# Kernel optimization log

Measured on AMD Instinct MI355X. Metric: run time of the kernel, lower is better.

The kernel has to match this reference:

```python
import math
import jax, jax.numpy as jnp
import numpy as np

D = 1536      # d_model
H = 12        # n_heads
L = 12        # n_layers
V = 50257     # vocab (hardcoded in module)
P = 1024      # max positions (hardcoded)
B = 1         # batch (must be 1: pos-embed uses arange(len(idx)))
S = 1024      # sequence length


def setup_inputs() -> dict:
    key = jax.random.key(0)
    ks = jax.random.split(key, 10)
    sc = 0.02
    n = lambda k, shape: (jax.random.normal(k, shape, jnp.float32) * sc)
    return {
        "idx": jax.random.randint(ks[0], (B, S), 0, V),
        "mask": jnp.tril(jnp.ones((S, S), jnp.int32)),  # causal mask
        "tok_emb": n(ks[1], (V, D)),
        "pos_emb": n(ks[2], (P, D)),
        "Wqkv": n(ks[3], (L, D, 3 * D)), "bqkv": jnp.zeros((L, 3 * D), jnp.float32),
        "Wo":   n(ks[4], (L, D, D)),     "bo":   jnp.zeros((L, D), jnp.float32),
        "W1":   n(ks[5], (L, D, 4 * D)), "b1":   jnp.zeros((L, 4 * D), jnp.float32),
        "W2":   n(ks[6], (L, 4 * D, D)), "b2":   jnp.zeros((L, D), jnp.float32),
        "ln_g": jnp.ones((D,), jnp.float32), "ln_b": jnp.zeros((D,), jnp.float32),
        "Wout": n(ks[7], (D, D)), "bout": jnp.zeros((D,), jnp.float32),
    }


def _gpt_forward(idx, mask, tok_emb, pos_emb, Wqkv, bqkv, Wo, bo,
                 W1, b1, W2, b2, ln_g, ln_b, Wout, bout):
    b, s = idx.shape
    d = tok_emb.shape[1]
    hd = d // H
    scale = 1.0 / math.sqrt(d)  # note: module divides by sqrt(d_model), not head_dim

    # faithful quirk: position_embedding(arange(len(idx))) -> (B, D), broadcasts since B==1
    x = tok_emb[idx] + pos_emb[:b]  # (B,S,D)

    mask0 = (mask == 0)  # (S,S) -> broadcast over (B,H,S,S)

    def block(x, p):
        wqkv, bqkv_, wo, bo_, w1, b1_, w2, b2_ = p
        qkv = x @ wqkv + bqkv_                       # (B,S,3D)
        q, k, v = jnp.split(qkv, 3, axis=-1)
        q = q.reshape(b, s, H, hd)
        k = k.reshape(b, s, H, hd)
        v = v.reshape(b, s, H, hd)
        scores = jnp.einsum('bqhd,bkhd->bhqk', q, k) * scale
        scores = jnp.where(mask0, -jnp.inf, scores)
        attn = jax.nn.softmax(scores, axis=-2)       # non-standard: softmax over QUERY axis
        o = jnp.einsum('bhqk,bkhd->bqhd', attn, v).reshape(b, s, d)
        x = x + (o @ wo + bo_)                       # attention residual
        x = x + (jax.nn.relu(x @ w1 + b1_) @ w2 + b2_)  # FFN residual (on post-attn x)
        return x, None

    x, _ = jax.lax.scan(block, x, (Wqkv, bqkv, Wo, bo, W1, b1, W2, b2))

    # final LayerNorm (eps=1e-5 like torch default)
    mu = jnp.mean(x, axis=-1, keepdims=True)
    var = jnp.mean(jnp.square(x - mu), axis=-1, keepdims=True)
    xn = (x - mu) * jax.lax.rsqrt(var + 1e-5) * ln_g + ln_b
    return xn @ Wout + bout


def reference(idx, mask, tok_emb, pos_emb, Wqkv, bqkv, Wo, bo,
              W1, b1, W2, b2, ln_g, ln_b, Wout, bout):
    return _gpt_forward(idx, mask, tok_emb, pos_emb, Wqkv, bqkv, Wo, bo,
                        W1, b1, W2, b2, ln_g, ln_b, Wout, bout)
```

## Files before the change

### kernel.cpp

```cpp
#include <hip/hip_runtime.h>
#include <stdint.h>
#include <math.h>

#define D_MODEL 1536
#define NH 12
#define HD 128
#define NL 12
#define SEQ 1024
#define D3 4608
#define D4 6144
#define SCALE 0.025515518153991442f

typedef __attribute__((ext_vector_type(8))) short short8;
typedef __attribute__((ext_vector_type(4))) float floatx4;

__device__ __forceinline__ uint32_t packhi(float a, float b) {
  return (__float_as_uint(a) >> 16) | (__float_as_uint(b) & 0xFFFF0000u);
}
__device__ __forceinline__ float truncf32(float a) {
  return __uint_as_float(__float_as_uint(a) & 0xFFFF0000u);
}
__device__ __forceinline__ void split8v(float4 v0, float4 v1, uint4 &hi, uint4 &lo) {
  hi.x = packhi(v0.x, v0.y); hi.y = packhi(v0.z, v0.w);
  hi.z = packhi(v1.x, v1.y); hi.w = packhi(v1.z, v1.w);
  lo.x = packhi(v0.x - truncf32(v0.x), v0.y - truncf32(v0.y));
  lo.y = packhi(v0.z - truncf32(v0.z), v0.w - truncf32(v0.w));
  lo.z = packhi(v1.x - truncf32(v1.x), v1.y - truncf32(v1.y));
  lo.w = packhi(v1.z - truncf32(v1.z), v1.w - truncf32(v1.w));
}

__device__ __forceinline__ int xcd_chunk_id(int nwg) {
  int orig = blockIdx.x;
  int xcd = orig & 7, pos = orig >> 3;
  int q = nwg >> 3, r = nwg & 7;
  return (xcd < r ? xcd * (q + 1) : r * (q + 1) + (xcd - r) * q) + pos;
}

__global__ __launch_bounds__(256)
void embed_kernel(const int* __restrict__ idx, const float* __restrict__ tok,
                  const float* __restrict__ pos, float* __restrict__ x) {
  int i = blockIdx.x * 256 + threadIdx.x;
  int s = i / D_MODEL;
  int d = i - s * D_MODEL;
  x[i] = tok[(size_t)idx[s] * D_MODEL + d] + pos[d];
}

template<int BM, bool RELU, bool RES, int SPLITK, bool TA2>
__global__ __launch_bounds__(256)
void mgemm_kernel(const float* __restrict__ A, const float* __restrict__ Ab,
                  const float* __restrict__ B,
                  const float* __restrict__ bias, const float* __restrict__ res,
                  float* __restrict__ C, int M, int N, int K, int NC, int NR) {
  constexpr int MI = BM / 32;
  constexpr int AE = BM / 8;
  constexpr int TPR = 32 / AE;
  __shared__ short Ah[2][BM][36], Al[2][BM][36];
  __shared__ short Bh[2][128][36], Bl[2][128][36];
  const int tid = threadIdx.x;
  const int lane = tid & 63, wave = tid >> 6;

  const int lid = xcd_chunk_id(NC * NR * SPLITK);
  const int z   = lid / (NC * NR);
  const int rem = lid - z * (NC * NR);
  const int ct  = rem / NR;
  const int rt  = rem - ct * NR;
  const int bm = rt * BM, bn = ct << 7;

  const int wm = (wave >> 1) * (BM / 2), wn = (wave & 1) << 6;
  const int fr = lane & 15, fk = (lane >> 4) << 3;
  const int Kc = K / SPLITK;
  const int kbase = (SPLITK > 1) ? z * Kc : 0;

  floatx4 acc[MI][4];
#pragma unroll
  for (int i = 0; i < MI; i++)
#pragma unroll
    for (int j = 0; j < 4; j++) acc[i][j] = (floatx4){0.f, 0.f, 0.f, 0.f};

  const int ar = tid / TPR;
  const int ac = (tid % TPR) * AE;
  const int bc = tid & 127;
  const int bkq = (tid >> 7) << 4;
  const float* Ag  = A + (size_t)(bm + ar) * K + kbase + ac;
  const float* Ag2 = TA2 ? (Ab + (size_t)(bm + ar) * K + kbase + ac) : nullptr;
  const float* Bg = B + (size_t)(kbase + bkq) * N + bn + bc;

  float a_reg[AE];
  float b_reg[16];

  auto LOADG = [&](int k0) {
#pragma unroll
    for (int e = 0; e < AE / 4; e++) {
      float4 v = *(const float4*)(Ag + k0 + 4 * e);
      if constexpr (TA2) {
        float4 w = *(const float4*)(Ag2 + k0 + 4 * e);
        v.x += w.x; v.y += w.y; v.z += w.z; v.w += w.w;
      }
      a_reg[4 * e + 0] = v.x; a_reg[4 * e + 1] = v.y;
      a_reg[4 * e + 2] = v.z; a_reg[4 * e + 3] = v.w;
    }
    const float* Bp = Bg + (size_t)k0 * N;
#pragma unroll
    for (int j = 0; j < 16; j++) b_reg[j] = Bp[(size_t)j * N];
  };
  auto STORE = [&](int buf) {
#pragma unroll
    for (int e = 0; e < AE / 8; e++) {
      float4 v0 = {a_reg[8 * e + 0], a_reg[8 * e + 1], a_reg[8 * e + 2], a_reg[8 * e + 3]};
      float4 v1 = {a_reg[8 * e + 4], a_reg[8 * e + 5], a_reg[8 * e + 6], a_reg[8 * e + 7]};
      uint4 hi, lo; split8v(v0, v1, hi, lo);
      *(uint4*)&Ah[buf][ar][ac + 8 * e] = hi;
      *(uint4*)&Al[buf][ar][ac + 8 * e] = lo;
    }
#pragma unroll
    for (int e = 0; e < 2; e++) {
      float4 u0 = {b_reg[8 * e + 0], b_reg[8 * e + 1], b_reg[8 * e + 2], b_reg[8 * e + 3]};
      float4 u1 = {b_reg[8 * e + 4], b_reg[8 * e + 5], b_reg[8 * e + 6], b_reg[8 * e + 7]};
      uint4 hi, lo; split8v(u0, u1, hi, lo);
      *(uint4*)&Bh[buf][bc][bkq + 8 * e] = hi;
      *(uint4*)&Bl[buf][bc][bkq + 8 * e] = lo;
    }
  };

  LOADG(0);
  STORE(0);
  __syncthreads();

  for (int k0 = 0; k0 < Kc; k0 += 32) {
    const int cur = (k0 >> 5) & 1;
    const bool more = (k0 + 32 < Kc);
    if (more) LOADG(k0 + 32);

    short8 ah[MI], al[MI], bh[4], bl[4];
#pragma unroll
    for (int i = 0; i < MI; i++) {
      ah[i] = *(const short8*)&Ah[cur][wm + (i << 4) + fr][fk];
      al[i] = *(const short8*)&Al[cur][wm + (i << 4) + fr][fk];
    }
#pragma unroll
    for (int j = 0; j < 4; j++) {
      bh[j] = *(const short8*)&Bh[cur][wn + (j << 4) + fr][fk];
      bl[j] = *(const short8*)&Bl[cur][wn + (j << 4) + fr][fk];
    }
#pragma unroll
    for (int i = 0; i < MI; i++)
#pragma unroll
      for (int j = 0; j < 4; j++) {
        acc[i][j] = __builtin_amdgcn_mfma_f32_16x16x32_bf16(ah[i], bh[j], acc[i][j], 0, 0, 0);
        acc[i][j] = __builtin_amdgcn_mfma_f32_16x16x32_bf16(ah[i], bl[j], acc[i][j], 0, 0, 0);
        acc[i][j] = __builtin_amdgcn_mfma_f32_16x16x32_bf16(al[i], bh[j], acc[i][j], 0, 0, 0);
      }

    if (more) STORE(cur ^ 1);
    __syncthreads();
  }

  const int cr = (lane >> 4) << 2, cc = lane & 15;
  if constexpr (SPLITK > 1) {
    float* Cp = C + (size_t)z * M * N;
#pragma unroll
    for (int j = 0; j < 4; j++) {
      const int col = bn + wn + (j << 4) + cc;
#pragma unroll
      for (int i = 0; i < MI; i++) {
        const int row0 = bm + wm + (i << 4) + cr;
#pragma unroll
        for (int r = 0; r < 4; r++)
          Cp[(size_t)(row0 + r) * N + col] = acc[i][j][r];
      }
    }
  } else {
#pragma unroll
    for (int j = 0; j < 4; j++) {
      const int col = bn + wn + (j << 4) + cc;
      const float bv = bias[col];
#pragma unroll
      for (int i = 0; i < MI; i++) {
        const int row0 = bm + wm + (i << 4) + cr;
#pragma unroll
        for (int r = 0; r < 4; r++) {
          float v = acc[i][j][r] + bv;
          if constexpr (RES) v += res[(size_t)(row0 + r) * N + col];
          if constexpr (RELU) v = fmaxf(v, 0.f);
          C[(size_t)(row0 + r) * N + col] = v;
        }
      }
    }
  }
}

template<bool HASB, bool RES, bool RELU>
__global__ __launch_bounds__(256)
void combine_kernel(const float* __restrict__ p0, const float* __restrict__ p1,
                    const float* __restrict__ bias, const float* __restrict__ res,
                    float* __restrict__ C, int N) {
  const int i = (blockIdx.x * 256 + threadIdx.x) << 2;
  float4 a = *(const float4*)&p0[i];
  float4 b = *(const float4*)&p1[i];
  float4 r = {a.x + b.x, a.y + b.y, a.z + b.z, a.w + b.w};
  if constexpr (HASB) {
    const int col = i % N;
    float4 bv = *(const float4*)&bias[col];
    r.x += bv.x; r.y += bv.y; r.z += bv.z; r.w += bv.w;
  }
  if constexpr (RES) {
    float4 rv = *(const float4*)&res[i];
    r.x += rv.x; r.y += rv.y; r.z += rv.z; r.w += rv.w;
  }
  if constexpr (RELU) {
    r.x = fmaxf(r.x, 0.f); r.y = fmaxf(r.y, 0.f);
    r.z = fmaxf(r.z, 0.f); r.w = fmaxf(r.w, 0.f);
  }
  *(float4*)&C[i] = r;
}

__global__ __launch_bounds__(256)
void scores_kernel(const float* __restrict__ qkv, float* __restrict__ scores,
                   float* __restrict__ pstats) {
  __shared__ short Qh[128][40], Ql[128][40], Kh[128][40], Kl[128][40];
  const int tid = threadIdx.x;
  const int lane = tid & 63, wave = tid >> 6;

  const int lid = xcd_chunk_id(NH * 36);
  const int h = lid / 36;
  int t = lid - h * 36;
  int rr = 0;
  while ((rr + 1) * (rr + 2) / 2 <= t) rr++;
  const int bi = rr << 7;
  const int bj = (t - rr * (rr + 1) / 2) << 7;

  const int wm = (wave >> 1) << 6, wn = (wave & 1) << 6;
  const int fr = lane & 15, fk = (lane >> 4) << 3;
  const float* Q = qkv + h * HD;
  const float* Kp = qkv + D_MODEL + h * HD;

  floatx4 acc[4][4];
#pragma unroll
  for (int i = 0; i < 4; i++)
#pragma unroll
    for (int j = 0; j < 4; j++) acc[i][j] = (floatx4){0.f, 0.f, 0.f, 0.f};

  const int ar = tid >> 1;
  const int ac = (tid & 1) << 4;

  for (int k0 = 0; k0 < HD; k0 += 32) {
    __syncthreads();
    {
      const float* Qp = Q + (size_t)(bi + ar) * D3 + k0 + ac;
#pragma unroll
      for (int e = 0; e < 2; e++) {
        float4 v0 = *(const float4*)(Qp + 8 * e);
        float4 v1 = *(const float4*)(Qp + 8 * e + 4);
        uint4 hi, lo; split8v(v0, v1, hi, lo);
        *(uint4*)&Qh[ar][ac + 8 * e] = hi;
        *(uint4*)&Ql[ar][ac + 8 * e] = lo;
      }
      const float* Kpp = Kp + (size_t)(bj + ar) * D3 + k0 + ac;
#pragma unroll
      for (int e = 0; e < 2; e++) {
        float4 v0 = *(const float4*)(Kpp + 8 * e);
        float4 v1 = *(const float4*)(Kpp + 8 * e + 4);
        uint4 hi, lo; split8v(v0, v1, hi, lo);
        *(uint4*)&Kh[ar][ac + 8 * e] = hi;
        *(uint4*)&Kl[ar][ac + 8 * e] = lo;
      }
    }
    __syncthreads();
    short8 qh[4], ql[4], kh[4], kl[4];
#pragma unroll
    for (int i = 0; i < 4; i++) {
      qh[i] = *(const short8*)&Qh[wm + (i << 4) + fr][fk];
      ql[i] = *(const short8*)&Ql[wm + (i << 4) + fr][fk];
      kh[i] = *(const short8*)&Kh[wn + (i << 4) + fr][fk];
      kl[i] = *(const short8*)&Kl[wn + (i << 4) + fr][fk];
    }
#pragma unroll
    for (int i = 0; i < 4; i++)
#pragma unroll
      for (int j = 0; j < 4; j++) {
        acc[i][j] = __builtin_amdgcn_mfma_f32_16x16x32_bf16(qh[i], kh[j], acc[i][j], 0, 0, 0);
        acc[i][j] = __builtin_amdgcn_mfma_f32_16x16x32_bf16(qh[i], kl[j], acc[i][j], 0, 0, 0);
        acc[i][j] = __builtin_amdgcn_mfma_f32_16x16x32_bf16(ql[i], kh[j], acc[i][j], 0, 0, 0);
        acc[i][j] = __builtin_amdgcn_mfma_f32_16x16x32_bf16(ql[i], kl[j], acc[i][j], 0, 0, 0);
      }
  }

  const int cr = (lane >> 4) << 2, cc = lane & 15;
  float* S = scores + (size_t)h * SEQ * SEQ;
  const int qc = (bi >> 6) + (wave >> 1);
  float* Pm = pstats + (size_t)((h * 16 + qc) * 2 + 0) * 1024;
  float* Pz = pstats + (size_t)((h * 16 + qc) * 2 + 1) * 1024;
#pragma unroll
  for (int j = 0; j < 4; j++) {
    const int col = bj + wn + (j << 4) + cc;
    float vv[16];
    float m = -1e30f;
#pragma unroll
    for (int i = 0; i < 4; i++) {
      const int row0 = bi + wm + (i << 4) + cr;
#pragma unroll
      for (int r = 0; r < 4; r++) {
        float v = (col <= row0 + r) ? acc[i][j][r] * SCALE : -1e30f;
        S[(size_t)(row0 + r) * SEQ + col] = v;
        vv[i * 4 + r] = v;
        m = fmaxf(m, v);
      }
    }
    float zz = 0.f;
#pragma unroll
    for (int t2 = 0; t2 < 16; t2++) zz += __expf(vv[t2] - m);
    if (m == -1e30f) zz = 0.f;
#pragma unroll
    for (int off = 16; off <= 32; off <<= 1) {
      float mo = __shfl_xor(m, off, 64);
      float zo = __shfl_xor(zz, off, 64);
      float mn = fmaxf(m, mo);
      zz = zz * __expf(m - mn) + zo * __expf(mo - mn);
      m = mn;
    }
    if ((lane >> 4) == 0) { Pm[col] = m; Pz[col] = zz; }
  }
}

__global__ __launch_bounds__(256)
void av_kernel(const float* __restrict__ qkv, const float* __restrict__ scores,
               const float* __restrict__ pstats, float* __restrict__ part) {
  __shared__ short Ph[64][40], Pl[64][40], Vh[128][40], Vl[128][40];
  __shared__ float Ms[512], Rs[512];
  const int tid = threadIdx.x;
  const int lane = tid & 63, wave = tid >> 6;

  const int lid = xcd_chunk_id(NH * 32);
  const int h = lid >> 5;
  const int t = lid & 31;
  const int y = t >> 1, z = t & 1;
  const int bm = y << 6;

  const int wm = (wave >> 1) << 5, wn = (wave & 1) << 6;
  const int fr = lane & 15, fk = (lane >> 4) << 3;
  const float* S = scores + (size_t)h * SEQ * SEQ;
  const float* V = qkv + 2 * D_MODEL + h * HD;

  const int kbeg = z * (y + 1) * 32;
  const int kend = (z + 1) * (y + 1) * 32;
  const int ncols = kend - kbeg;

  for (int c0 = tid; c0 < ncols; c0 += 256) {
    const int c = kbeg + c0;
    const int q0 = c >> 6;
    float m = -1e30f;
    for (int qc = q0; qc < 16; qc++)
      m = fmaxf(m, pstats[(size_t)((h * 16 + qc) * 2 + 0) * 1024 + c]);
    float zz = 0.f;
    for (int qc = q0; qc < 16; qc++) {
      float pm = pstats[(size_t)((h * 16 + qc) * 2 + 0) * 1024 + c];
      float pz = pstats[(size_t)((h * 16 + qc) * 2 + 1) * 1024 + c];
      zz += pz * __expf(pm - m);
    }
    Ms[c0] = m;
    Rs[c0] = 1.f / zz;
  }

  floatx4 acc[2][4];
#pragma unroll
  for (int i = 0; i < 2; i++)
#pragma unroll
    for (int j = 0; j < 4; j++) acc[i][j] = (floatx4){0.f, 0.f, 0.f, 0.f};

  const int ar = tid >> 2;
  const int ac = (tid & 3) << 3;
  const int bc = tid & 127;
  const int bkq = (tid >> 7) << 4;

  for (int k0 = kbeg; k0 < kend; k0 += 32) {
    __syncthreads();
    {
      const float* Sp = S + (size_t)(bm + ar) * SEQ + k0 + ac;
      float4 v0 = *(const float4*)(Sp);
      float4 v1 = *(const float4*)(Sp + 4);
      float t8[8] = {v0.x, v0.y, v0.z, v0.w, v1.x, v1.y, v1.z, v1.w};
      float4 p0, p1;
      {
        int kk = k0 - kbeg + ac;
        p0.x = __expf(t8[0] - Ms[kk + 0]) * Rs[kk + 0];
        p0.y = __expf(t8[1] - Ms[kk + 1]) * Rs[kk + 1];
        p0.z = __expf(t8[2] - Ms[kk + 2]) * Rs[kk + 2];
        p0.w = __expf(t8[3] - Ms[kk + 3]) * Rs[kk + 3];
        p1.x = __expf(t8[4] - Ms[kk + 4]) * Rs[kk + 4];
        p1.y = __expf(t8[5] - Ms[kk + 5]) * Rs[kk + 5];
        p1.z = __expf(t8[6] - Ms[kk + 6]) * Rs[kk + 6];
        p1.w = __expf(t8[7] - Ms[kk + 7]) * Rs[kk + 7];
      }
      uint4 hi, lo; split8v(p0, p1, hi, lo);
      *(uint4*)&Ph[ar][ac] = hi;
      *(uint4*)&Pl[ar][ac] = lo;
    }
    {
      const float* Vp = V + (size_t)(k0 + bkq) * D3 + bc;
#pragma unroll
      for (int e = 0; e < 2; e++) {
        float4 u0, u1;
        u0.x = Vp[(size_t)(8 * e + 0) * D3]; u0.y = Vp[(size_t)(8 * e + 1) * D3];
        u0.z = Vp[(size_t)(8 * e + 2) * D3]; u0.w = Vp[(size_t)(8 * e + 3) * D3];
        u1.x = Vp[(size_t)(8 * e + 4) * D3]; u1.y = Vp[(size_t)(8 * e + 5) * D3];
        u1.z = Vp[(size_t)(8 * e + 6) * D3]; u1.w = Vp[(size_t)(8 * e + 7) * D3];
        uint4 hi, lo; split8v(u0, u1, hi, lo);
        *(uint4*)&Vh[bc][bkq + 8 * e] = hi;
        *(uint4*)&Vl[bc][bkq + 8 * e] = lo;
      }
    }
    __syncthreads();
    short8 ph[2], pl[2], vh[4], vl[4];
#pragma unroll
    for (int i = 0; i < 2; i++) {
      ph[i] = *(const short8*)&Ph[wm + (i << 4) + fr][fk];
      pl[i] = *(const short8*)&Pl[wm + (i << 4) + fr][fk];
    }
#pragma unroll
    for (int j = 0; j < 4; j++) {
      vh[j] = *(const short8*)&Vh[wn + (j << 4) + fr][fk];
      vl[j] = *(const short8*)&Vl[wn + (j << 4) + fr][fk];
    }
#pragma unroll
    for (int i = 0; i < 2; i++)
#pragma unroll
      for (int j = 0; j < 4; j++) {
        acc[i][j] = __builtin_amdgcn_mfma_f32_16x16x32_bf16(ph[i], vh[j], acc[i][j], 0, 0, 0);
        acc[i][j] = __builtin_amdgcn_mfma_f32_16x16x32_bf16(ph[i], vl[j], acc[i][j], 0, 0, 0);
        acc[i][j] = __builtin_amdgcn_mfma_f32_16x16x32_bf16(pl[i], vh[j], acc[i][j], 0, 0, 0);
      }
  }

  const int cr = (lane >> 4) << 2, cc = lane & 15;
  float* Cp = part + (size_t)z * SEQ * D_MODEL;
#pragma unroll
  for (int j = 0; j < 4; j++) {
    const int col = h * HD + wn + (j << 4) + cc;
#pragma unroll
    for (int i = 0; i < 2; i++) {
      const int row0 = bm + wm + (i << 4) + cr;
#pragma unroll
      for (int r = 0; r < 4; r++)
        Cp[(size_t)(row0 + r) * D_MODEL + col] = acc[i][j][r];
    }
  }
}

__global__ __launch_bounds__(256)
void ln_kernel(const float* __restrict__ x, const float* __restrict__ g,
               const float* __restrict__ bb, float* __restrict__ y) {
  __shared__ float red[8];
  const int row = blockIdx.x;
  const float* xr = x + (size_t)row * D_MODEL;
  float v[6];
  float s = 0.f, sq = 0.f;
#pragma unroll
  for (int i = 0; i < 6; i++) {
    v[i] = xr[256 * i + threadIdx.x];
    s += v[i];
    sq += v[i] * v[i];
  }
#pragma unroll
  for (int off = 32; off >= 1; off >>= 1) {
    s += __shfl_down(s, off, 64);
    sq += __shfl_down(sq, off, 64);
  }
  const int lane = threadIdx.x & 63, w = threadIdx.x >> 6;
  if (lane == 0) { red[w] = s; red[4 + w] = sq; }
  __syncthreads();
  if (threadIdx.x == 0) {
    red[0] = red[0] + red[1] + red[2] + red[3];
    red[4] = red[4] + red[5] + red[6] + red[7];
  }
  __syncthreads();
  const float mu = red[0] * (1.f / D_MODEL);
  const float var = red[4] * (1.f / D_MODEL) - mu * mu;
  const float rs = rsqrtf(var + 1e-5f);
#pragma unroll
  for (int i = 0; i < 6; i++) {
    int c = 256 * i + threadIdx.x;
    y[(size_t)row * D_MODEL + c] = (v[i] - mu) * rs * g[c] + bb[c];
  }
}

extern "C" void kernel_launch(void* const* d_in, const int* in_sizes, int n_in,
                              void* d_out, int out_size, void* d_ws, size_t ws_size,
                              hipStream_t stream) {
  (void)in_sizes; (void)n_in; (void)out_size; (void)ws_size;
  const int*   idx     = (const int*)d_in[0];
  const float* tok_emb = (const float*)d_in[2];
  const float* pos_emb = (const float*)d_in[3];
  const float* Wqkv    = (const float*)d_in[4];
  const float* bqkv    = (const float*)d_in[5];
  const float* Wo      = (const float*)d_in[6];
  const float* bo      = (const float*)d_in[7];
  const float* W1      = (const float*)d_in[8];
  const float* b1      = (const float*)d_in[9];
  const float* W2      = (const float*)d_in[10];
  const float* b2      = (const float*)d_in[11];
  const float* ln_g    = (const float*)d_in[12];
  const float* ln_b    = (const float*)d_in[13];
  const float* Wout    = (const float*)d_in[14];
  const float* bout    = (const float*)d_in[15];
  float* out = (float*)d_out;

  char* ws = (char*)d_ws;
  float* x      = (float*)(ws);
  float* qkv    = (float*)(ws + 6291456);
  float* pstats = (float*)(ws + 25165824);
  float* part   = (float*)(ws + 26836992);
  float* U      = (float*)(ws + 52002816);
  float* scores = U;
  float* h1     = U;
  float* xn     = U;
  const size_t PN = (size_t)SEQ * D_MODEL;

  embed_kernel<<<6144, 256, 0, stream>>>(idx, tok_emb, pos_emb, x);

  for (int l = 0; l < NL; l++) {
    const float* wqkv = Wqkv + (size_t)l * D_MODEL * D3;
    const float* bq   = bqkv + (size_t)l * D3;
    const float* wo   = Wo   + (size_t)l * D_MODEL * D_MODEL;
    const float* bo_  = bo   + (size_t)l * D_MODEL;
    const float* w1   = W1   + (size_t)l * D_MODEL * D4;
    const float* b1_  = b1   + (size_t)l * D4;
    const float* w2   = W2   + (size_t)l * D4 * D_MODEL;
    const float* b2_  = b2   + (size_t)l * D_MODEL;

    mgemm_kernel<128, false, false, 1, false><<<288, 256, 0, stream>>>(
        x, nullptr, wqkv, bq, nullptr, qkv, SEQ, D3, D_MODEL, 36, 8);
    scores_kernel<<<432, 256, 0, stream>>>(qkv, scores, pstats);
    av_kernel<<<384, 256, 0, stream>>>(qkv, scores, pstats, part);
    mgemm_kernel<64, false, false, 2, true><<<384, 256, 0, stream>>>(
        part, part + PN, wo, nullptr, nullptr, part + 2 * PN,
        SEQ, D_MODEL, D_MODEL, 12, 16);
    combine_kernel<true, true, false><<<1536, 256, 0, stream>>>(
        part + 2 * PN, part + 3 * PN, bo_, x, x, D_MODEL);
    mgemm_kernel<128, true, false, 1, false><<<384, 256, 0, stream>>>(
        x, nullptr, w1, b1_, nullptr, h1, SEQ, D4, D_MODEL, 48, 8);
    mgemm_kernel<64, false, false, 2, false><<<384, 256, 0, stream>>>(
        h1, nullptr, w2, nullptr, nullptr, part, SEQ, D_MODEL, D4, 12, 16);
    combine_kernel<true, true, false><<<1536, 256, 0, stream>>>(
        part, part + PN, b2_, x, x, D_MODEL);
  }

  ln_kernel<<<SEQ, 256, 0, stream>>>(x, ln_g, ln_b, xn);
  mgemm_kernel<64, false, false, 2, false><<<384, 256, 0, stream>>>(
      xn, nullptr, Wout, nullptr, nullptr, part, SEQ, D_MODEL, D_MODEL, 12, 16);
  combine_kernel<true, false, false><<<1536, 256, 0, stream>>>(
      part, part + PN, bout, nullptr, out, D_MODEL);
}
```

Measured before the change: 5.060 ms.

## Load A/Q/K/P MFMA fragments directly from global into registers, bypassing LDS

In the GEMM, scores and AV kernels, the row-major operand (A, Q/K, P) is now read from global memory straight into the per-lane MFMA fragment layout and split into bf16 hi/lo in registers, removing the LDS staging buffers. The scores kernel drops its barriers entirely. This saves shared-memory traffic, LDS capacity and syncs. In exchange, each wave redundantly loads A rows that other waves also need, and the global access pattern becomes less coalesced (16 rows by 32 bytes per fragment), which leans on L1/L2 hit rates.

```diff
diff --git a/kernel.cpp b/kernel.cpp
--- a/kernel.cpp
+++ b/kernel.cpp
@@ -28,6 +28,9 @@
   lo.z = packhi(v1.x - truncf32(v1.x), v1.y - truncf32(v1.y));
   lo.w = packhi(v1.z - truncf32(v1.z), v1.w - truncf32(v1.w));
 }
+__device__ __forceinline__ short8 u4s8(uint4 u) {
+  union { uint4 u; short8 s; } x; x.u = u; return x.s;
+}
 
 __device__ __forceinline__ int xcd_chunk_id(int nwg) {
   int orig = blockIdx.x;
@@ -52,9 +55,6 @@
                   const float* __restrict__ bias, const float* __restrict__ res,
                   float* __restrict__ C, int M, int N, int K, int NC, int NR) {
   constexpr int MI = BM / 32;
-  constexpr int AE = BM / 8;
-  constexpr int TPR = 32 / AE;
-  __shared__ short Ah[2][BM][36], Al[2][BM][36];
   __shared__ short Bh[2][128][36], Bl[2][128][36];
   const int tid = threadIdx.x;
   const int lane = tid & 63, wave = tid >> 6;
@@ -77,41 +77,27 @@
 #pragma unroll
     for (int j = 0; j < 4; j++) acc[i][j] = (floatx4){0.f, 0.f, 0.f, 0.f};
 
-  const int ar = tid / TPR;
-  const int ac = (tid % TPR) * AE;
   const int bc = tid & 127;
   const int bkq = (tid >> 7) << 4;
-  const float* Ag  = A + (size_t)(bm + ar) * K + kbase + ac;
-  const float* Ag2 = TA2 ? (Ab + (size_t)(bm + ar) * K + kbase + ac) : nullptr;
   const float* Bg = B + (size_t)(kbase + bkq) * N + bn + bc;
-
-  float a_reg[AE];
   float b_reg[16];
 
-  auto LOADG = [&](int k0) {
-#pragma unroll
-    for (int e = 0; e < AE / 4; e++) {
-      float4 v = *(const float4*)(Ag + k0 + 4 * e);
-      if constexpr (TA2) {
-        float4 w = *(const float4*)(Ag2 + k0 + 4 * e);
-        v.x += w.x; v.y += w.y; v.z += w.z; v.w += w.w;
-      }
-      a_reg[4 * e + 0] = v.x; a_reg[4 * e + 1] = v.y;
-      a_reg[4 * e + 2] = v.z; a_reg[4 * e + 3] = v.w;
-    }
+  const float* Aq[MI];
+  const float* Aq2[MI];
+#pragma unroll
+  for (int i = 0; i < MI; i++) {
+    Aq[i] = A + (size_t)(bm + wm + 16 * i + fr) * K + kbase + fk;
+    if constexpr (TA2) Aq2[i] = Ab + (size_t)(bm + wm + 16 * i + fr) * K + kbase + fk;
+  }
+
+  float4 a0c[MI], a1c[MI], a0n[MI], a1n[MI];
+
+  auto LOADB = [&](int k0) {
     const float* Bp = Bg + (size_t)k0 * N;
 #pragma unroll
     for (int j = 0; j < 16; j++) b_reg[j] = Bp[(size_t)j * N];
   };
-  auto STORE = [&](int buf) {
-#pragma unroll
-    for (int e = 0; e < AE / 8; e++) {
-      float4 v0 = {a_reg[8 * e + 0], a_reg[8 * e + 1], a_reg[8 * e + 2], a_reg[8 * e + 3]};
-      float4 v1 = {a_reg[8 * e + 4], a_reg[8 * e + 5], a_reg[8 * e + 6], a_reg[8 * e + 7]};
-      uint4 hi, lo; split8v(v0, v1, hi, lo);
-      *(uint4*)&Ah[buf][ar][ac + 8 * e] = hi;
-      *(uint4*)&Al[buf][ar][ac + 8 * e] = lo;
-    }
+  auto STOREB = [&](int buf) {
 #pragma unroll
     for (int e = 0; e < 2; e++) {
       float4 u0 = {b_reg[8 * e + 0], b_reg[8 * e + 1], b_reg[8 * e + 2], b_reg[8 * e + 3]};
@@ -121,21 +107,39 @@
       *(uint4*)&Bl[buf][bc][bkq + 8 * e] = lo;
     }
   };
-
-  LOADG(0);
-  STORE(0);
+  auto LOADA = [&](int k0, float4* d0, float4* d1) {
+#pragma unroll
+    for (int i = 0; i < MI; i++) {
+      float4 v0 = *(const float4*)(Aq[i] + k0);
+      float4 v1 = *(const float4*)(Aq[i] + k0 + 4);
+      if constexpr (TA2) {
+        float4 w0 = *(const float4*)(Aq2[i] + k0);
+        float4 w1 = *(const float4*)(Aq2[i] + k0 + 4);
+        v0.x += w0.x; v0.y += w0.y; v0.z += w0.z; v0.w += w0.w;
+        v1.x += w1.x; v1.y += w1.y; v1.z += w1.z; v1.w += w1.w;
+      }
+      d0[i] = v0; d1[i] = v1;
+    }
+  };
+
+  LOADB(0);
+  STOREB(0);
+  LOADA(0, a0c, a1c);
   __syncthreads();
 
   for (int k0 = 0; k0 < Kc; k0 += 32) {
     const int cur = (k0 >> 5) & 1;
     const bool more = (k0 + 32 < Kc);
-    if (more) LOADG(k0 + 32);
+    if (more) {
+      LOADB(k0 + 32);
+      LOADA(k0 + 32, a0n, a1n);
+    }
 
     short8 ah[MI], al[MI], bh[4], bl[4];
 #pragma unroll
     for (int i = 0; i < MI; i++) {
-      ah[i] = *(const short8*)&Ah[cur][wm + (i << 4) + fr][fk];
-      al[i] = *(const short8*)&Al[cur][wm + (i << 4) + fr][fk];
+      uint4 hi, lo; split8v(a0c[i], a1c[i], hi, lo);
+      ah[i] = u4s8(hi); al[i] = u4s8(lo);
     }
 #pragma unroll
     for (int j = 0; j < 4; j++) {
@@ -151,7 +155,11 @@
         acc[i][j] = __builtin_amdgcn_mfma_f32_16x16x32_bf16(al[i], bh[j], acc[i][j], 0, 0, 0);
       }
 
-    if (more) STORE(cur ^ 1);
+    if (more) {
+      STOREB(cur ^ 1);
+#pragma unroll
+      for (int i = 0; i < MI; i++) { a0c[i] = a0n[i]; a1c[i] = a1n[i]; }
+    }
     __syncthreads();
   }
 
@@ -217,7 +225,6 @@
 __global__ __launch_bounds__(256)
 void scores_kernel(const float* __restrict__ qkv, float* __restrict__ scores,
                    float* __restrict__ pstats) {
-  __shared__ short Qh[128][40], Ql[128][40], Kh[128][40], Kl[128][40];
   const int tid = threadIdx.x;
   const int lane = tid & 63, wave = tid >> 6;
 
@@ -231,8 +238,6 @@
 
   const int wm = (wave >> 1) << 6, wn = (wave & 1) << 6;
   const int fr = lane & 15, fk = (lane >> 4) << 3;
-  const float* Q = qkv + h * HD;
-  const float* Kp = qkv + D_MODEL + h * HD;
 
   floatx4 acc[4][4];
 #pragma unroll
@@ -240,39 +245,27 @@
 #pragma unroll
     for (int j = 0; j < 4; j++) acc[i][j] = (floatx4){0.f, 0.f, 0.f, 0.f};
 
-  const int ar = tid >> 1;
-  const int ac = (tid & 1) << 4;
-
+  const float* Qp[4];
+  const float* Kp[4];
+#pragma unroll
+  for (int i = 0; i < 4; i++) {
+    Qp[i] = qkv + h * HD + (size_t)(bi + wm + 16 * i + fr) * D3 + fk;
+    Kp[i] = qkv + D_MODEL + h * HD + (size_t)(bj + wn + 16 * i + fr) * D3 + fk;
+  }
+
+#pragma unroll
   for (int k0 = 0; k0 < HD; k0 += 32) {
-    __syncthreads();
-    {
-      const float* Qp = Q + (size_t)(bi + ar) * D3 + k0 + ac;
-#pragma unroll
-      for (int e = 0; e < 2; e++) {
-        float4 v0 = *(const float4*)(Qp + 8 * e);
-        float4 v1 = *(const float4*)(Qp + 8 * e + 4);
-        uint4 hi, lo; split8v(v0, v1, hi, lo);
-        *(uint4*)&Qh[ar][ac + 8 * e] = hi;
-        *(uint4*)&Ql[ar][ac + 8 * e] = lo;
-      }
-      const float* Kpp = Kp + (size_t)(bj + ar) * D3 + k0 + ac;
-#pragma unroll
-      for (int e = 0; e < 2; e++) {
-        float4 v0 = *(const float4*)(Kpp + 8 * e);
-        float4 v1 = *(const float4*)(Kpp + 8 * e + 4);
-        uint4 hi, lo; split8v(v0, v1, hi, lo);
-        *(uint4*)&Kh[ar][ac + 8 * e] = hi;
-        *(uint4*)&Kl[ar][ac + 8 * e] = lo;
-      }
-    }
-    __syncthreads();
     short8 qh[4], ql[4], kh[4], kl[4];
 #pragma unroll
     for (int i = 0; i < 4; i++) {
-      qh[i] = *(const short8*)&Qh[wm + (i << 4) + fr][fk];
-      ql[i] = *(const short8*)&Ql[wm + (i << 4) + fr][fk];
-      kh[i] = *(const short8*)&Kh[wn + (i << 4) + fr][fk];
-      kl[i] = *(const short8*)&Kl[wn + (i << 4) + fr][fk];
+      float4 v0 = *(const float4*)(Qp[i] + k0);
+      float4 v1 = *(const float4*)(Qp[i] + k0 + 4);
+      uint4 hi, lo; split8v(v0, v1, hi, lo);
+      qh[i] = u4s8(hi); ql[i] = u4s8(lo);
+      float4 w0 = *(const float4*)(Kp[i] + k0);
+      float4 w1 = *(const float4*)(Kp[i] + k0 + 4);
+      split8v(w0, w1, hi, lo);
+      kh[i] = u4s8(hi); kl[i] = u4s8(lo);
     }
 #pragma unroll
     for (int i = 0; i < 4; i++)
@@ -325,7 +318,7 @@
 __global__ __launch_bounds__(256)
 void av_kernel(const float* __restrict__ qkv, const float* __restrict__ scores,
                const float* __restrict__ pstats, float* __restrict__ part) {
-  __shared__ short Ph[64][40], Pl[64][40], Vh[128][40], Vl[128][40];
+  __shared__ short Vh[128][40], Vl[128][40];
   __shared__ float Ms[512], Rs[512];
   const int tid = threadIdx.x;
   const int lane = tid & 63, wave = tid >> 6;
@@ -367,34 +360,11 @@
 #pragma unroll
     for (int j = 0; j < 4; j++) acc[i][j] = (floatx4){0.f, 0.f, 0.f, 0.f};
 
-  const int ar = tid >> 2;
-  const int ac = (tid & 3) << 3;
   const int bc = tid & 127;
   const int bkq = (tid >> 7) << 4;
 
   for (int k0 = kbeg; k0 < kend; k0 += 32) {
     __syncthreads();
-    {
-      const float* Sp = S + (size_t)(bm + ar) * SEQ + k0 + ac;
-      float4 v0 = *(const float4*)(Sp);
-      float4 v1 = *(const float4*)(Sp + 4);
-      float t8[8] = {v0.x, v0.y, v0.z, v0.w, v1.x, v1.y, v1.z, v1.w};
-      float4 p0, p1;
-      {
-        int kk = k0 - kbeg + ac;
-        p0.x = __expf(t8[0] - Ms[kk + 0]) * Rs[kk + 0];
-        p0.y = __expf(t8[1] - Ms[kk + 1]) * Rs[kk + 1];
-        p0.z = __expf(t8[2] - Ms[kk + 2]) * Rs[kk + 2];
-        p0.w = __expf(t8[3] - Ms[kk + 3]) * Rs[kk + 3];
-        p1.x = __expf(t8[4] - Ms[kk + 4]) * Rs[kk + 4];
-        p1.y = __expf(t8[5] - Ms[kk + 5]) * Rs[kk + 5];
-        p1.z = __expf(t8[6] - Ms[kk + 6]) * Rs[kk + 6];
-        p1.w = __expf(t8[7] - Ms[kk + 7]) * Rs[kk + 7];
-      }
-      uint4 hi, lo; split8v(p0, p1, hi, lo);
-      *(uint4*)&Ph[ar][ac] = hi;
-      *(uint4*)&Pl[ar][ac] = lo;
-    }
     {
       const float* Vp = V + (size_t)(k0 + bkq) * D3 + bc;
 #pragma unroll
@@ -409,13 +379,28 @@
         *(uint4*)&Vl[bc][bkq + 8 * e] = lo;
       }
     }
+    short8 ph[2], pl[2];
+#pragma unroll
+    for (int i = 0; i < 2; i++) {
+      const int row = bm + wm + (i << 4) + fr;
+      const float* Sp = S + (size_t)row * SEQ + k0 + fk;
+      float4 s0 = *(const float4*)(Sp);
+      float4 s1 = *(const float4*)(Sp + 4);
+      const int kk = k0 - kbeg + fk;
+      float4 p0, p1;
+      p0.x = __expf(s0.x - Ms[kk + 0]) * Rs[kk + 0];
+      p0.y = __expf(s0.y - Ms[kk + 1]) * Rs[kk + 1];
+      p0.z = __expf(s0.z - Ms[kk + 2]) * Rs[kk + 2];
+      p0.w = __expf(s0.w - Ms[kk + 3]) * Rs[kk + 3];
+      p1.x = __expf(s1.x - Ms[kk + 4]) * Rs[kk + 4];
+      p1.y = __expf(s1.y - Ms[kk + 5]) * Rs[kk + 5];
+      p1.z = __expf(s1.z - Ms[kk + 6]) * Rs[kk + 6];
+      p1.w = __expf(s1.w - Ms[kk + 7]) * Rs[kk + 7];
+      uint4 hi, lo; split8v(p0, p1, hi, lo);
+      ph[i] = u4s8(hi); pl[i] = u4s8(lo);
+    }
     __syncthreads();
-    short8 ph[2], pl[2], vh[4], vl[4];
-#pragma unroll
-    for (int i = 0; i < 2; i++) {
-      ph[i] = *(const short8*)&Ph[wm + (i << 4) + fr][fk];
-      pl[i] = *(const short8*)&Pl[wm + (i << 4) + fr][fk];
-    }
+    short8 vh[4], vl[4];
 #pragma unroll
     for (int j = 0; j < 4; j++) {
       vh[j] = *(const short8*)&Vh[wn + (j << 4) + fr][fk];
```

New measurement: 6.201 ms. +22.6%, slower.
